# Kernel tuning notes

Hardware: AMD Instinct MI355X
Metric: run time of the kernel (lower is better)

The kernel has to match this reference:

```python
import jax, jax.numpy as jnp
import numpy as np


def _pairwise_dist(x, y):
    # x: [B, N, D], y: [B, M, D] -> [B, N, M] Euclidean distances.
    # Use ||x||^2 + ||y||^2 - 2<x,y> (gram form) to avoid the [B,N,M,D]
    # broadcast intermediate the torch code materializes.
    x2 = jnp.sum(x * x, axis=-1)  # [B, N]
    y2 = jnp.sum(y * y, axis=-1)  # [B, M]
    xy = jnp.einsum('bnd,bmd->bnm', x, y)  # [B, N, M]
    sq = x2[:, :, None] + y2[:, None, :] - 2.0 * xy
    return jnp.sqrt(jnp.maximum(sq, 1e-12))


def setup_inputs() -> dict:
    key = jax.random.key(0)
    k1, k2 = jax.random.split(key)
    B, N, M, D = 8, 4096, 4096, 64
    pred = jax.random.normal(k1, (B, N, D), dtype=jnp.float32)
    label = jax.random.normal(k2, (B, M, D), dtype=jnp.float32)
    return {"pred": pred, "label": label}


def reference(pred, label):
    dis = _pairwise_dist(pred, label)  # [B, N, M]
    dis_xy = jnp.max(jnp.min(dis, axis=2))  # max over all (b, n) of min over m
    dis_yx = jnp.max(jnp.min(dis, axis=1))  # max over all (b, m) of min over n
    return dis_xy + dis_yx
```

## Files before the change

### kernel.cpp

```cpp
#include <hip/hip_runtime.h>
#include <hip/hip_bf16.h>

#define B_ 8
#define N_ 4096
#define M_ 4096
#define D_ 64
#define BNT (B_ * N_)
#define BMT (B_ * M_)
#define TA 64
#define TB 64
#define CHUNK_TILES 16
#define MCHUNK (M_ / (TB * CHUNK_TILES))

typedef short bf16x8 __attribute__((ext_vector_type(8)));
typedef float f32x4 __attribute__((ext_vector_type(4)));

__device__ __forceinline__ unsigned short f2bf(float f) {
  __hip_bfloat16 h = __float2bfloat16(f);
  return *reinterpret_cast<unsigned short*>(&h);
}

__device__ __forceinline__ unsigned fkey(float f) {
  unsigned b = __float_as_uint(f);
  return b ^ ((unsigned)((int)b >> 31) | 0x80000000u);
}
__device__ __forceinline__ float funkey(unsigned k) {
  unsigned b = (k & 0x80000000u) ? (k ^ 0x80000000u) : ~k;
  return __uint_as_float(b);
}

__device__ __forceinline__ void gload_lds16(const void* g, void* l) {
  __builtin_amdgcn_global_load_lds(
      (const __attribute__((address_space(1))) unsigned int*)g,
      (__attribute__((address_space(3))) unsigned int*)l, 16, 0, 0);
}

template <int ROWS, bool BF>
__device__ __forceinline__ void stage_tile(const void* gsrc, unsigned short* lds,
                                           int t, int srcpat) {
  if (BF) {
    constexpr int PER_WAVE = (ROWS * 128 / 1024) / 4;
    const char* gp = (const char*)gsrc;
    int w = t >> 6;
#pragma unroll
    for (int i = 0; i < PER_WAVE; i++) {
      int q = w * PER_WAVE + i;
      gload_lds16(gp + q * 1024 + srcpat, (char*)lds + q * 1024);
    }
  } else {
    const float4* g4 = (const float4*)gsrc;
#pragma unroll
    for (int i = 0; i < ROWS * 16 / 256; i++) {
      int off = i * 256 + t;
      float4 v = g4[off];
      int row = off >> 4;
      int cb = (off & 15) * 8;
      int ba = (row * 128 + cb) ^ ((row & 7) << 4);
      ushort4 p;
      p.x = f2bf(v.x); p.y = f2bf(v.y); p.z = f2bf(v.z); p.w = f2bf(v.w);
      *(ushort4*)((char*)lds + ba) = p;
    }
  }
}

template <bool CONV>
__global__ __launch_bounds__(256) void prep_kernel(
    const float* __restrict__ pred, const float* __restrict__ label,
    unsigned short* __restrict__ predbf, unsigned short* __restrict__ labelbf,
    float* __restrict__ x2, float* __restrict__ y2,
    unsigned* __restrict__ minN, unsigned* __restrict__ minM) {
  int t = threadIdx.x;
  int lane = t & 15;
  long row = (long)blockIdx.x * 16 + (t >> 4);
  const float4* src;
  unsigned short* bdst;
  float* ndst;
  unsigned* mdst;
  if (row < BNT) {
    src = (const float4*)(pred + row * D_);
    bdst = predbf + row * D_;
    ndst = x2 + row;
    mdst = minN + row;
  } else {
    long r2 = row - BNT;
    src = (const float4*)(label + r2 * D_);
    bdst = labelbf + r2 * D_;
    ndst = y2 + r2;
    mdst = minM + r2;
  }
  float4 v = src[lane];
  if (CONV) {
    ushort4 p;
    p.x = f2bf(v.x); p.y = f2bf(v.y); p.z = f2bf(v.z); p.w = f2bf(v.w);
    *(ushort4*)(bdst + lane * 4) = p;
  }
  float s = v.x * v.x + v.y * v.y + v.z * v.z + v.w * v.w;
  s += __shfl_xor(s, 1);
  s += __shfl_xor(s, 2);
  s += __shfl_xor(s, 4);
  s += __shfl_xor(s, 8);
  if (lane == 0) {
    *ndst = s;
    *mdst = 0xFFFFFFFFu;
  }
}

template <bool BF>
__global__ __launch_bounds__(256) void fused_kernel(
    const void* __restrict__ Asrc, const void* __restrict__ Bsrc,
    const float* __restrict__ x2g, const float* __restrict__ y2g,
    unsigned* __restrict__ minN, unsigned* __restrict__ minM) {
  __shared__ alignas(16) unsigned short As[TA * 64];
  __shared__ alignas(16) unsigned short Bs[2][TB * 64];
  __shared__ float red[4][TA];

  const int t = threadIdx.x;
  const int b = blockIdx.z;
  const int a0 = blockIdx.x * TA;
  const int tile0 = blockIdx.y * CHUNK_TILES;
  const int w = t >> 6, l = t & 63;
  const int g = l >> 4, c = l & 15;
  const int srcpat = (l >> 3) * 128 + (((l & 7) * 16) ^ ((l >> 3) << 4));

  const size_t rowbytes = BF ? 128 : 256;
  const char* Agl = (const char*)Asrc + ((size_t)b * N_ + a0) * rowbytes;
  const char* Bgl = (const char*)Bsrc + (size_t)b * M_ * rowbytes;

  float y2v[CHUNK_TILES];
  {
    const float* yb = y2g + (size_t)b * M_ + tile0 * TB + w * 16 + c;
#pragma unroll
    for (int it = 0; it < CHUNK_TILES; it++) y2v[it] = yb[it * TB];
  }

  stage_tile<TA, BF>(Agl, As, t, srcpat);
  stage_tile<TB, BF>(Bgl + (size_t)tile0 * TB * rowbytes, Bs[0], t, srcpat);
  __syncthreads();

  bf16x8 af[2][4];
#pragma unroll
  for (int kk = 0; kk < 2; kk++)
#pragma unroll
    for (int mi = 0; mi < 4; mi++) {
      int r = mi * 16 + c;
      int ba = (r * 128 + kk * 64 + g * 16) ^ ((r & 7) << 4);
      af[kk][mi] = *(const bf16x8*)((const char*)As + ba);
    }

  float x2v[4][4];
#pragma unroll
  for (int mi = 0; mi < 4; mi++)
#pragma unroll
    for (int e = 0; e < 4; e++)
      x2v[mi][e] = x2g[(size_t)b * N_ + a0 + mi * 16 + g * 4 + e];

  float rmin[4][4];
#pragma unroll
  for (int mi = 0; mi < 4; mi++)
#pragma unroll
    for (int e = 0; e < 4; e++) rmin[mi][e] = INFINITY;

#pragma unroll
  for (int it = 0; it < CHUNK_TILES; it++) {
    if (it + 1 < CHUNK_TILES)
      stage_tile<TB, BF>(Bgl + (size_t)(tile0 + it + 1) * TB * rowbytes,
                         Bs[(it + 1) & 1], t, srcpat);
    const char* Bcur = (const char*)Bs[it & 1];

    int r = w * 16 + c;
    bf16x8 b0 = *(const bf16x8*)(Bcur + ((r * 128 + g * 16) ^ ((r & 7) << 4)));
    bf16x8 b1 = *(const bf16x8*)(Bcur + ((r * 128 + 64 + g * 16) ^ ((r & 7) << 4)));
    f32x4 acc[4];
#pragma unroll
    for (int mi = 0; mi < 4; mi++)
      acc[mi] = __builtin_amdgcn_mfma_f32_16x16x32_bf16(
          af[0][mi], b0, (f32x4){0.f, 0.f, 0.f, 0.f}, 0, 0, 0);
#pragma unroll
    for (int mi = 0; mi < 4; mi++)
      acc[mi] = __builtin_amdgcn_mfma_f32_16x16x32_bf16(
          af[1][mi], b1, acc[mi], 0, 0, 0);

    float nbv = y2v[it];
    float cm = INFINITY;
#pragma unroll
    for (int mi = 0; mi < 4; mi++)
#pragma unroll
      for (int e = 0; e < 4; e++) {
        rmin[mi][e] = fminf(rmin[mi][e], fmaf(-2.f, acc[mi][e], nbv));
        cm = fminf(cm, fmaf(-2.f, acc[mi][e], x2v[mi][e]));
      }
    cm = fminf(cm, __shfl_xor(cm, 16));
    cm = fminf(cm, __shfl_xor(cm, 32));
    if (g == 0)
      atomicMin(&minM[(size_t)b * M_ + (tile0 + it) * TB + w * 16 + c], fkey(cm));

    __syncthreads();
  }

#pragma unroll
  for (int mi = 0; mi < 4; mi++)
#pragma unroll
    for (int e = 0; e < 4; e++) {
      float r = rmin[mi][e];
      r = fminf(r, __shfl_xor(r, 1));
      r = fminf(r, __shfl_xor(r, 2));
      r = fminf(r, __shfl_xor(r, 4));
      r = fminf(r, __shfl_xor(r, 8));
      rmin[mi][e] = r;
    }
  if (c == 0) {
#pragma unroll
    for (int mi = 0; mi < 4; mi++)
#pragma unroll
      for (int e = 0; e < 4; e++)
        red[w][mi * 16 + g * 4 + e] = rmin[mi][e];
  }
  __syncthreads();
  if (t < TA) {
    float m = fminf(fminf(red[0][t], red[1][t]), fminf(red[2][t], red[3][t]));
    atomicMin(&minN[(size_t)b * N_ + a0 + t], fkey(m));
  }
}

__global__ __launch_bounds__(1024) void final_kernel(
    const unsigned* __restrict__ minN, const unsigned* __restrict__ minM,
    const float* __restrict__ x2, const float* __restrict__ y2,
    float* __restrict__ out) {
  int t = threadIdx.x;
  int dir = t >> 9;
  int i0 = t & 511;
  const unsigned* src = dir ? minM : minN;
  const float* nrm = dir ? y2 : x2;
  float mx = -INFINITY;
  for (int i = i0; i < BNT / 4; i += 512) {
    uint4 k = ((const uint4*)src)[i];
    float4 nv = ((const float4*)nrm)[i];
    mx = fmaxf(mx, nv.x + funkey(k.x));
    mx = fmaxf(mx, nv.y + funkey(k.y));
    mx = fmaxf(mx, nv.z + funkey(k.z));
    mx = fmaxf(mx, nv.w + funkey(k.w));
  }
#pragma unroll
  for (int mask = 1; mask < 64; mask <<= 1) mx = fmaxf(mx, __shfl_xor(mx, mask));
  __shared__ float sm[16];
  if ((t & 63) == 0) sm[t >> 6] = mx;
  __syncthreads();
  if (t == 0) {
    float a = -INFINITY, bm = -INFINITY;
#pragma unroll
    for (int i = 0; i < 8; i++) {
      a = fmaxf(a, sm[i]);
      bm = fmaxf(bm, sm[8 + i]);
    }
    out[0] = sqrtf(fmaxf(a, 1e-12f)) + sqrtf(fmaxf(bm, 1e-12f));
  }
}

extern "C" void kernel_launch(void* const* d_in, const int* in_sizes, int n_in,
                              void* d_out, int out_size, void* d_ws, size_t ws_size,
                              hipStream_t stream) {
  const float* pred = (const float*)d_in[0];
  const float* label = (const float*)d_in[1];
  char* ws = (char*)d_ws;

  const size_t bfBytes = (size_t)BNT * D_ * 2;
  const size_t needFast = 2 * bfBytes + (size_t)(BNT + BMT) * 8 + 64;

  if (ws_size >= needFast) {
    unsigned short* predbf = (unsigned short*)ws;
    unsigned short* labelbf = (unsigned short*)(ws + bfBytes);
    float* x2 = (float*)(ws + 2 * bfBytes);
    float* y2 = x2 + BNT;
    unsigned* minN = (unsigned*)(y2 + BMT);
    unsigned* minM = minN + BNT;

    prep_kernel<true><<<(BNT + BMT) / 16, 256, 0, stream>>>(
        pred, label, predbf, labelbf, x2, y2, minN, minM);
    fused_kernel<true><<<dim3(N_ / TA, MCHUNK, B_), 256, 0, stream>>>(
        predbf, labelbf, x2, y2, minN, minM);
    final_kernel<<<1, 1024, 0, stream>>>(minN, minM, x2, y2, (float*)d_out);
  } else {
    float* x2 = (float*)ws;
    float* y2 = x2 + BNT;
    unsigned* minN = (unsigned*)(y2 + BMT);
    unsigned* minM = minN + BNT;

    prep_kernel<false><<<(BNT + BMT) / 16, 256, 0, stream>>>(
        pred, label, nullptr, nullptr, x2, y2, minN, minM);
    fused_kernel<false><<<dim3(N_ / TA, MCHUNK, B_), 256, 0, stream>>>(
        pred, label, x2, y2, minN, minM);
    final_kernel<<<1, 1024, 0, stream>>>(minN, minM, x2, y2, (float*)d_out);
  }
}
```

Measured before the change: 67.35 us.

## Load MFMA operands directly from global and batch column-min atomics via LDS

Drops the LDS staging of A and B tiles, including the double buffer, global_load_lds and per-iteration __syncthreads. Each lane now loads its bf16x8 fragments straight from global, or converts them from fp32. Per-tile column minima are written to an LDS buffer and flushed with one coalesced pass of atomicMin at the end, instead of issuing atomics every iteration. This removes barriers and staging overhead, but the loads become uncoalesced at row stride with less explicit prefetch, relying on caches to absorb the reuse.

After: 72.81 us. +8.1%, slower.

```diff
diff --git a/kernel.cpp b/kernel.cpp
--- a/kernel.cpp
+++ b/kernel.cpp
@@ -10,7 +10,8 @@
 #define TA 64
 #define TB 64
 #define CHUNK_TILES 16
-#define MCHUNK (M_ / (TB * CHUNK_TILES))
+#define CHUNK_B (TB * CHUNK_TILES)
+#define MCHUNK (M_ / CHUNK_B)
 
 typedef short bf16x8 __attribute__((ext_vector_type(8)));
 typedef float f32x4 __attribute__((ext_vector_type(4)));
@@ -29,38 +30,11 @@
   return __uint_as_float(b);
 }
 
-__device__ __forceinline__ void gload_lds16(const void* g, void* l) {
-  __builtin_amdgcn_global_load_lds(
-      (const __attribute__((address_space(1))) unsigned int*)g,
-      (__attribute__((address_space(3))) unsigned int*)l, 16, 0, 0);
-}
-
-template <int ROWS, bool BF>
-__device__ __forceinline__ void stage_tile(const void* gsrc, unsigned short* lds,
-                                           int t, int srcpat) {
-  if (BF) {
-    constexpr int PER_WAVE = (ROWS * 128 / 1024) / 4;
-    const char* gp = (const char*)gsrc;
-    int w = t >> 6;
-#pragma unroll
-    for (int i = 0; i < PER_WAVE; i++) {
-      int q = w * PER_WAVE + i;
-      gload_lds16(gp + q * 1024 + srcpat, (char*)lds + q * 1024);
-    }
-  } else {
-    const float4* g4 = (const float4*)gsrc;
-#pragma unroll
-    for (int i = 0; i < ROWS * 16 / 256; i++) {
-      int off = i * 256 + t;
-      float4 v = g4[off];
-      int row = off >> 4;
-      int cb = (off & 15) * 8;
-      int ba = (row * 128 + cb) ^ ((row & 7) << 4);
-      ushort4 p;
-      p.x = f2bf(v.x); p.y = f2bf(v.y); p.z = f2bf(v.z); p.w = f2bf(v.w);
-      *(ushort4*)((char*)lds + ba) = p;
-    }
-  }
+__device__ __forceinline__ bf16x8 cvt8(float4 lo, float4 hi) {
+  union { unsigned short u[8]; bf16x8 v; } r;
+  r.u[0] = f2bf(lo.x); r.u[1] = f2bf(lo.y); r.u[2] = f2bf(lo.z); r.u[3] = f2bf(lo.w);
+  r.u[4] = f2bf(hi.x); r.u[5] = f2bf(hi.y); r.u[6] = f2bf(hi.z); r.u[7] = f2bf(hi.w);
+  return r.v;
 }
 
 template <bool CONV>
@@ -110,42 +84,36 @@
     const void* __restrict__ Asrc, const void* __restrict__ Bsrc,
     const float* __restrict__ x2g, const float* __restrict__ y2g,
     unsigned* __restrict__ minN, unsigned* __restrict__ minM) {
-  __shared__ alignas(16) unsigned short As[TA * 64];
-  __shared__ alignas(16) unsigned short Bs[2][TB * 64];
+  __shared__ float cmLDS[CHUNK_B];
   __shared__ float red[4][TA];
 
   const int t = threadIdx.x;
   const int b = blockIdx.z;
   const int a0 = blockIdx.x * TA;
-  const int tile0 = blockIdx.y * CHUNK_TILES;
+  const int row0 = blockIdx.y * CHUNK_B;
   const int w = t >> 6, l = t & 63;
   const int g = l >> 4, c = l & 15;
-  const int srcpat = (l >> 3) * 128 + (((l & 7) * 16) ^ ((l >> 3) << 4));
-
-  const size_t rowbytes = BF ? 128 : 256;
-  const char* Agl = (const char*)Asrc + ((size_t)b * N_ + a0) * rowbytes;
-  const char* Bgl = (const char*)Bsrc + (size_t)b * M_ * rowbytes;
-
-  float y2v[CHUNK_TILES];
-  {
-    const float* yb = y2g + (size_t)b * M_ + tile0 * TB + w * 16 + c;
-#pragma unroll
-    for (int it = 0; it < CHUNK_TILES; it++) y2v[it] = yb[it * TB];
-  }
-
-  stage_tile<TA, BF>(Agl, As, t, srcpat);
-  stage_tile<TB, BF>(Bgl + (size_t)tile0 * TB * rowbytes, Bs[0], t, srcpat);
-  __syncthreads();
 
   bf16x8 af[2][4];
-#pragma unroll
-  for (int kk = 0; kk < 2; kk++)
-#pragma unroll
-    for (int mi = 0; mi < 4; mi++) {
-      int r = mi * 16 + c;
-      int ba = (r * 128 + kk * 64 + g * 16) ^ ((r & 7) << 4);
-      af[kk][mi] = *(const bf16x8*)((const char*)As + ba);
-    }
+  if (BF) {
+    const unsigned short* Ab =
+        (const unsigned short*)Asrc + ((size_t)b * N_ + a0) * D_;
+#pragma unroll
+    for (int kk = 0; kk < 2; kk++)
+#pragma unroll
+      for (int mi = 0; mi < 4; mi++)
+        af[kk][mi] = *(const bf16x8*)(Ab + (mi * 16 + c) * D_ + kk * 32 + g * 8);
+  } else {
+    const float* Af = (const float*)Asrc + ((size_t)b * N_ + a0) * D_;
+#pragma unroll
+    for (int kk = 0; kk < 2; kk++)
+#pragma unroll
+      for (int mi = 0; mi < 4; mi++) {
+        const float4* p =
+            (const float4*)(Af + (mi * 16 + c) * D_ + kk * 32 + g * 8);
+        af[kk][mi] = cvt8(p[0], p[1]);
+      }
+  }
 
   float x2v[4][4];
 #pragma unroll
@@ -160,16 +128,25 @@
 #pragma unroll
     for (int e = 0; e < 4; e++) rmin[mi][e] = INFINITY;
 
-#pragma unroll
+  const unsigned short* Bb = (const unsigned short*)Bsrc + ((size_t)b * M_ + row0) * D_;
+  const float* Bf = (const float*)Bsrc + ((size_t)b * M_ + row0) * D_;
+  const float* yb = y2g + (size_t)b * M_ + row0;
+
+#pragma unroll 4
   for (int it = 0; it < CHUNK_TILES; it++) {
-    if (it + 1 < CHUNK_TILES)
-      stage_tile<TB, BF>(Bgl + (size_t)(tile0 + it + 1) * TB * rowbytes,
-                         Bs[(it + 1) & 1], t, srcpat);
-    const char* Bcur = (const char*)Bs[it & 1];
-
-    int r = w * 16 + c;
-    bf16x8 b0 = *(const bf16x8*)(Bcur + ((r * 128 + g * 16) ^ ((r & 7) << 4)));
-    bf16x8 b1 = *(const bf16x8*)(Bcur + ((r * 128 + 64 + g * 16) ^ ((r & 7) << 4)));
+    const int r = it * TB + w * 16 + c;
+    float nbv = yb[r];
+    bf16x8 b0, b1;
+    if (BF) {
+      b0 = *(const bf16x8*)(Bb + (size_t)r * D_ + g * 8);
+      b1 = *(const bf16x8*)(Bb + (size_t)r * D_ + 32 + g * 8);
+    } else {
+      const float4* p0 = (const float4*)(Bf + (size_t)r * D_ + g * 8);
+      const float4* p1 = (const float4*)(Bf + (size_t)r * D_ + 32 + g * 8);
+      b0 = cvt8(p0[0], p0[1]);
+      b1 = cvt8(p1[0], p1[1]);
+    }
+
     f32x4 acc[4];
 #pragma unroll
     for (int mi = 0; mi < 4; mi++)
@@ -180,7 +157,6 @@
       acc[mi] = __builtin_amdgcn_mfma_f32_16x16x32_bf16(
           af[1][mi], b1, acc[mi], 0, 0, 0);
 
-    float nbv = y2v[it];
     float cm = INFINITY;
 #pragma unroll
     for (int mi = 0; mi < 4; mi++)
@@ -191,10 +167,7 @@
       }
     cm = fminf(cm, __shfl_xor(cm, 16));
     cm = fminf(cm, __shfl_xor(cm, 32));
-    if (g == 0)
-      atomicMin(&minM[(size_t)b * M_ + (tile0 + it) * TB + w * 16 + c], fkey(cm));
-
-    __syncthreads();
+    if (g == 0) cmLDS[r] = cm;
   }
 
 #pragma unroll
@@ -219,6 +192,11 @@
   if (t < TA) {
     float m = fminf(fminf(red[0][t], red[1][t]), fminf(red[2][t], red[3][t]));
     atomicMin(&minN[(size_t)b * N_ + a0 + t], fkey(m));
+  }
+#pragma unroll
+  for (int i = 0; i < CHUNK_B / 256; i++) {
+    int r = i * 256 + t;
+    atomicMin(&minM[(size_t)b * M_ + row0 + r], fkey(cmLDS[r]));
   }
 }
 
```
